# Performance work log

Hardware: AMD Instinct MI355X
Metric: run time of the kernel (lower is better)

## Reference

```python
import jax, jax.numpy as jnp
import numpy as np

N, E = 20000, 160000
D_NODE_IN, D_EDGE_IN = 256, 64
D = 128          # node/edge feature dim
H = 256          # edge hidden dim
T = 17           # number of keypoint types
EDGE_STEPS, NODE_STEPS = 2, 1


def _w(k, shape):
    return jax.random.normal(k, shape, dtype=jnp.float32) / np.sqrt(shape[-2] if len(shape) > 1 else shape[-1]).astype(np.float32)


def setup_inputs() -> dict:
    key = jax.random.key(0)
    ks = iter(jax.random.split(key, 40))
    inp = {
        'x': jax.random.normal(next(ks), (N, D_NODE_IN), dtype=jnp.float32),
        'edge_attr': jax.random.normal(next(ks), (E, D_EDGE_IN), dtype=jnp.float32),
        'edge_index': jax.random.randint(next(ks), (2, E), 0, N),
        'node_types': jax.random.randint(next(ks), (N,), 0, T),
        # type-routed node embedding: 17 stacked 2-layer MLPs 256->128->128
        'ne_w1': _w(next(ks), (T, D_NODE_IN, D)), 'ne_b1': jnp.zeros((T, D)),
        'ne_w2': _w(next(ks), (T, D, D)),         'ne_b2': jnp.zeros((T, D)),
        # edge embedding 64->128->128
        'ee_w1': _w(next(ks), (D_EDGE_IN, D)), 'ee_b1': jnp.zeros((D,)),
        'ee_w2': _w(next(ks), (D, D)),         'ee_b2': jnp.zeros((D,)),
        # MPLayer edge MLP: [x_i, x_j, e] with skip -> (2*2D + 2D)=768 -> 256 -> 128
        'me_w1': _w(next(ks), (4 * D + 2 * D, H)), 'me_b1': jnp.zeros((H,)),
        'me_w2': _w(next(ks), (H, D)),             'me_b2': jnp.zeros((D,)),
        # MPLayer node update: [x(skip 2D), agg(D)] -> 128
        'mn_w1': _w(next(ks), (2 * D + D, D)), 'mn_b1': jnp.zeros((D,)),
        # classifiers
        'ec_w1': _w(next(ks), (D, D)), 'ec_b1': jnp.zeros((D,)),
        'ec_w2': _w(next(ks), (D, 1)), 'ec_b2': jnp.zeros((1,)),
        'nc_w1': _w(next(ks), (D, D)), 'nc_b1': jnp.zeros((D,)),
        'nc_w2': _w(next(ks), (D, 1)), 'nc_b2': jnp.zeros((1,)),
        'cc_w1': _w(next(ks), (D, D)), 'cc_b1': jnp.zeros((D,)),
        'cc_w2': _w(next(ks), (D, T)), 'cc_b2': jnp.zeros((T,)),
    }
    return inp


def _mlp2(x, w1, b1, w2, b2):
    return jax.nn.relu(x @ w1 + b1) @ w2 + b2


def reference(x, edge_attr, edge_index, node_types,
              ne_w1, ne_b1, ne_w2, ne_b2,
              ee_w1, ee_b1, ee_w2, ee_b2,
              me_w1, me_b1, me_w2, me_b2,
              mn_w1, mn_b1,
              ec_w1, ec_b1, ec_w2, ec_b2,
              nc_w1, nc_b1, nc_w2, nc_b2,
              cc_w1, cc_b1, cc_w2, cc_b2):
    n = x.shape[0]
    # NodeMlpType: run all 17 MLPs, select by node type (same math as masked dispatch)
    h = jax.nn.relu(jnp.einsum('nd,tdk->tnk', x, ne_w1) + ne_b1[:, None, :])   # [T,N,D]
    o = jnp.einsum('tnk,tkm->tnm', h, ne_w2) + ne_b2[:, None, :]               # [T,N,D]
    nf0 = o[node_types, jnp.arange(n)]                                          # [N,D]
    ef0 = _mlp2(edge_attr, ee_w1, ee_b1, ee_w2, ee_b2)                          # [E,D]

    src, dst = edge_index[0], edge_index[1]

    def mp_step(nf, ef):
        nf_c = jnp.concatenate([nf0, nf], axis=1)                               # skip concat [N,2D]
        ef_c = jnp.concatenate([ef0, ef], axis=1)                               # [E,2D]
        m = jnp.concatenate([nf_c[dst], nf_c[src], ef_c], axis=1)               # [E,6D]
        e_new = _mlp2(m, me_w1, me_b1, me_w2, me_b2)                            # [E,D]
        agg = jax.ops.segment_sum(e_new, dst, num_segments=n)                   # aggr='add'
        nf_new = jnp.concatenate([nf_c, agg], axis=1) @ mn_w1 + mn_b1           # [N,D]
        return nf_new, e_new

    nf, ef = nf0, ef0
    for _ in range(EDGE_STEPS):
        nf, ef = mp_step(nf, ef)
    pred_edge = _mlp2(ef, ec_w1, ec_b1, ec_w2, ec_b2).squeeze(-1)               # [E]
    for _ in range(NODE_STEPS):
        nf, ef = mp_step(nf, ef)
    pred_node = _mlp2(nf, nc_w1, nc_b1, nc_w2, nc_b2).squeeze(-1)               # [N]
    pred_class = _mlp2(nf, cc_w1, cc_b1, cc_w2, cc_b2)                          # [N,T]
    return (pred_edge, pred_node, pred_class, nf, ef)
```

## Files before the change

### kernel.cpp

```cpp
#include <hip/hip_runtime.h>
#include <hip/hip_bf16.h>

#define N_NODES 20000
#define N_EDGES 160000
#define DIN_NODE 256
#define DIN_EDGE 64
#define DF 128
#define HH 256
#define TT 17
#define NE_PAD_SLOTS 20544
#define NB_NODE (NE_PAD_SLOTS / 32)

typedef __attribute__((ext_vector_type(8))) short short8v;
typedef __attribute__((ext_vector_type(4))) float f32x4;

__device__ __forceinline__ unsigned short f2bf(float f) {
  unsigned int u = __builtin_bit_cast(unsigned int, f);
  u += 0x7FFFu + ((u >> 16) & 1u);
  return (unsigned short)(u >> 16);
}

__device__ __forceinline__ float bf2f(unsigned short u) {
  return __builtin_bit_cast(float, (unsigned int)u << 16);
}

__device__ __forceinline__ short8v pack8(float4 a, float4 b) {
  short8v o;
  o[0] = (short)f2bf(a.x); o[1] = (short)f2bf(a.y);
  o[2] = (short)f2bf(a.z); o[3] = (short)f2bf(a.w);
  o[4] = (short)f2bf(b.x); o[5] = (short)f2bf(b.y);
  o[6] = (short)f2bf(b.z); o[7] = (short)f2bf(b.w);
  return o;
}

struct PackPtrs {
  const float *s0, *s1, *s2, *s3, *s4, *s5, *s6, *s7, *s8, *s9, *s10, *s11;
  unsigned short *d0, *d1, *d2, *d3, *d4, *d5, *d6, *d7, *d8, *d9, *d10, *d11;
};

__global__ __launch_bounds__(256) void k_pack_all(PackPtrs P) {
  const int g = blockIdx.x * 4 + (threadIdx.x >> 6);
  const int l = threadIdx.x & 63;
  if (g >= 2320) return;
  const float* w; unsigned short* out; int K, N, tile;
  if (g < 128)       { w = P.s0;  out = P.d0;  K = 256; N = 256; tile = g; }
  else if (g < 256)  { w = P.s1;  out = P.d1;  K = 256; N = 256; tile = g - 128; }
  else if (g < 384)  { w = P.s2;  out = P.d2;  K = 256; N = 256; tile = g - 256; }
  else if (g < 448)  { w = P.s3;  out = P.d3;  K = 256; N = 128; tile = g - 384; }
  else if (g < 544)  { w = P.s4;  out = P.d4;  K = 384; N = 128; tile = g - 448; }
  else if (g < 1632) { w = P.s5;  out = P.d5;  K = 256; N = 128; tile = g - 544; }
  else if (g < 2176) { w = P.s6;  out = P.d6;  K = 128; N = 128; tile = g - 1632; }
  else if (g < 2192) { w = P.s7;  out = P.d7;  K = 64;  N = 128; tile = g - 2176; }
  else if (g < 2224) { w = P.s8;  out = P.d8;  K = 128; N = 128; tile = g - 2192; }
  else if (g < 2256) { w = P.s9;  out = P.d9;  K = 128; N = 128; tile = g - 2224; }
  else if (g < 2288) { w = P.s10; out = P.d10; K = 128; N = 128; tile = g - 2256; }
  else               { w = P.s11; out = P.d11; K = 128; N = 128; tile = g - 2288; }
  const int ntTiles = N >> 4;
  const int tilesPer = (K >> 5) * ntTiles;
  const int bt = tile / tilesPer;
  const int rr = tile - bt * tilesPer;
  const int kt = rr / ntTiles, nt = rr - kt * ntTiles;
  const float* wb = w + (size_t)bt * K * N;
  const int col = (nt << 4) + (l & 15);
  const int k0 = (kt << 5) + ((l >> 4) << 3);
  unsigned short* o = out + (((size_t)tile << 6) + l) * 8;
#pragma unroll
  for (int j = 0; j < 8; ++j) o[j] = f2bf(wb[(size_t)(k0 + j) * N + col]);
}

__global__ void k_count_deg(const int* __restrict__ types,
                            const int* __restrict__ dstv,
                            int* __restrict__ cnt, int* __restrict__ deg) {
  const int i = blockIdx.x * 256 + threadIdx.x;
  if (i < N_NODES) atomicAdd(&cnt[types[i]], 1);
  if (i < N_EDGES) atomicAdd(&deg[dstv[i]], 1);
}

__global__ __launch_bounds__(256) void k_prefix_scan(
    const int* __restrict__ cnt, int* __restrict__ woff,
    const int* __restrict__ deg, int* __restrict__ rs, int* __restrict__ wo) {
  __shared__ int partial[256];
  const int t = threadIdx.x;
  if (t == 0) {
    int cur = 0;
    for (int ty = 0; ty < TT; ++ty) {
      woff[ty] = cur;
      cur += (cnt[ty] + 31) & ~31;
    }
  }
  const int base = t * 80;
  int s = 0;
  for (int j = 0; j < 80; ++j) {
    const int n = base + j;
    if (n < N_NODES) s += deg[n];
  }
  partial[t] = s;
  __syncthreads();
  for (int off = 1; off < 256; off <<= 1) {
    const int v = (t >= off) ? partial[t - off] : 0;
    __syncthreads();
    partial[t] += v;
    __syncthreads();
  }
  int run = (t > 0) ? partial[t - 1] : 0;
  for (int j = 0; j < 80; ++j) {
    const int n = base + j;
    if (n < N_NODES) {
      rs[n] = run; wo[n] = run;
      run += deg[n];
    }
  }
  if (t == 255) rs[N_NODES] = run;
}

__global__ void k_scatter_elist(const int* __restrict__ types,
                                const int* __restrict__ srcv,
                                const int* __restrict__ dstv,
                                int* __restrict__ woff, int* __restrict__ wo,
                                int* __restrict__ bucket,
                                int* __restrict__ elist, int* __restrict__ ipos,
                                int* __restrict__ srcp, int* __restrict__ dstp) {
  const int i = blockIdx.x * 256 + threadIdx.x;
  if (i < N_NODES) {
    const int pos = atomicAdd(&woff[types[i]], 1);
    bucket[pos] = i;
  }
  if (i < N_EDGES) {
    const int pos = atomicAdd(&wo[dstv[i]], 1);
    elist[pos] = i;
    ipos[i] = pos;
    srcp[pos] = srcv[i];
    dstp[pos] = dstv[i];
  }
}

__global__ __launch_bounds__(256) void k_embed_fused(
    const float* __restrict__ x, const int* __restrict__ bucket,
    const int* __restrict__ types,
    const unsigned short* __restrict__ wp1, const float* __restrict__ b1,
    const unsigned short* __restrict__ wp2, const float* __restrict__ b2,
    unsigned short* __restrict__ nf0b,
    const unsigned short* __restrict__ wpd, const unsigned short* __restrict__ wps,
    unsigned short* __restrict__ PDo, unsigned short* __restrict__ PSo,
    const float* __restrict__ ea, const int* __restrict__ ipos,
    const unsigned short* __restrict__ ewp1, const float* __restrict__ eb1,
    const unsigned short* __restrict__ ewp2, const float* __restrict__ eb2,
    unsigned short* __restrict__ ef0p) {
  __shared__ __align__(16) unsigned char A[32 * 512];
  __shared__ __align__(16) unsigned char Hb[32 * 256];
  __shared__ int sidx[32];
  const int t = threadIdx.x;
  const int w = t >> 6, l = t & 63, lr = l & 15, lg = l >> 4;
  const int sw = (lr & 7) << 4;
  const int row0 = lr, row1 = 16 + lr;

  if (blockIdx.x < NB_NODE) {
    const int r0 = blockIdx.x * 32;
    if (t < 32) sidx[t] = bucket[r0 + t];
    __syncthreads();
    if (sidx[0] < 0) return;
    const int ty = types[sidx[0]];

#pragma unroll
    for (int j = 0; j < 4; ++j) {
      const int q = j * 256 + t;
      const int i = q >> 5, c = q & 31;
      const int nd = sidx[i];
      short8v o;
      if (nd >= 0) {
        const float* xr = x + (size_t)nd * DIN_NODE + c * 8;
        o = pack8(*reinterpret_cast<const float4*>(xr),
                  *reinterpret_cast<const float4*>(xr + 4));
      } else {
#pragma unroll
        for (int k = 0; k < 8; ++k) o[k] = 0;
      }
      *reinterpret_cast<short8v*>(A + ((i * 512 + c * 16) ^ ((i & 7) << 4))) = o;
    }
    __syncthreads();

    f32x4 acc[2][2];
#pragma unroll
    for (int mt = 0; mt < 2; ++mt)
#pragma unroll
      for (int q = 0; q < 2; ++q)
#pragma unroll
        for (int r = 0; r < 4; ++r) acc[mt][q][r] = 0.f;
#pragma unroll
    for (int kt = 0; kt < 8; ++kt) {
      const short8v a0 = *reinterpret_cast<const short8v*>(
          A + ((row0 * 512 + kt * 64 + lg * 16) ^ sw));
      const short8v a1 = *reinterpret_cast<const short8v*>(
          A + ((row1 * 512 + kt * 64 + lg * 16) ^ sw));
#pragma unroll
      for (int q = 0; q < 2; ++q) {
// ... 104 lines not shown
    {
      const int i = t >> 3, c = t & 7;
      const float* xr = ea + (size_t)(e0 + i) * DIN_EDGE + c * 8;
      const short8v o = pack8(*reinterpret_cast<const float4*>(xr),
                              *reinterpret_cast<const float4*>(xr + 4));
      *reinterpret_cast<short8v*>(A + ((i * 128 + c * 16) ^ ((i & 7) << 4))) = o;
    }
    __syncthreads();

    f32x4 acc[2][2];
#pragma unroll
    for (int mt = 0; mt < 2; ++mt)
#pragma unroll
      for (int q = 0; q < 2; ++q)
#pragma unroll
        for (int r = 0; r < 4; ++r) acc[mt][q][r] = 0.f;
#pragma unroll
    for (int kt = 0; kt < 2; ++kt) {
      const short8v a0 = *reinterpret_cast<const short8v*>(
          A + ((row0 * 128 + kt * 64 + lg * 16) ^ sw));
      const short8v a1 = *reinterpret_cast<const short8v*>(
          A + ((row1 * 128 + kt * 64 + lg * 16) ^ sw));
#pragma unroll
      for (int q = 0; q < 2; ++q) {
        const short8v bq = *reinterpret_cast<const short8v*>(
            ewp1 + (((size_t)(kt * 8 + 2 * w + q) * 64 + l) << 3));
        acc[0][q] = __builtin_amdgcn_mfma_f32_16x16x32_bf16(a0, bq, acc[0][q], 0, 0, 0);
        acc[1][q] = __builtin_amdgcn_mfma_f32_16x16x32_bf16(a1, bq, acc[1][q], 0, 0, 0);
      }
    }
#pragma unroll
    for (int q = 0; q < 2; ++q) {
      const int col = (2 * w + q) * 16 + lr;
      const float bias = eb1[col];
#pragma unroll
      for (int mt = 0; mt < 2; ++mt)
#pragma unroll
        for (int r = 0; r < 4; ++r) {
          const int row = mt * 16 + lg * 4 + r;
          *reinterpret_cast<unsigned short*>(
              Hb + ((row * 256 + col * 2) ^ ((row & 7) << 4))) =
              f2bf(fmaxf(acc[mt][q][r] + bias, 0.f));
        }
    }
    __syncthreads();

    f32x4 acc2[2][2];
#pragma unroll
    for (int mt = 0; mt < 2; ++mt)
#pragma unroll
      for (int q = 0; q < 2; ++q)
#pragma unroll
        for (int r = 0; r < 4; ++r) acc2[mt][q][r] = 0.f;
#pragma unroll
    for (int kt = 0; kt < 4; ++kt) {
      const short8v a0 = *reinterpret_cast<const short8v*>(
          Hb + ((row0 * 256 + kt * 64 + lg * 16) ^ sw));
      const short8v a1 = *reinterpret_cast<const short8v*>(
          Hb + ((row1 * 256 + kt * 64 + lg * 16) ^ sw));
#pragma unroll
      for (int q = 0; q < 2; ++q) {
        const short8v bq = *reinterpret_cast<const short8v*>(
            ewp2 + (((size_t)(kt * 8 + 2 * w + q) * 64 + l) << 3));
        acc2[0][q] = __builtin_amdgcn_mfma_f32_16x16x32_bf16(a0, bq, acc2[0][q], 0, 0, 0);
        acc2[1][q] = __builtin_amdgcn_mfma_f32_16x16x32_bf16(a1, bq, acc2[1][q], 0, 0, 0);
      }
    }
#pragma unroll
    for (int q = 0; q < 2; ++q) {
      const int col = (2 * w + q) * 16 + lr;
      const float bias = eb2[col];
#pragma unroll
      for (int mt = 0; mt < 2; ++mt)
#pragma unroll
        for (int r = 0; r < 4; ++r) {
          const int row = mt * 16 + lg * 4 + r;
          ef0p[(size_t)sidx[row] * DF + col] = f2bf(acc2[mt][q][r] + bias);
        }
    }
  }
}

template <bool OUTF, bool HEAD>
__global__ __launch_bounds__(256, 4) void k_edge_mlp_mfma(
    const unsigned short* __restrict__ ef0, const unsigned short* __restrict__ ef_in,
    unsigned short* __restrict__ ef_out, float* __restrict__ ef_outf,
    const int* __restrict__ srcp, const int* __restrict__ dstp,
    const int* __restrict__ elist,
    const unsigned short* __restrict__ wpe, const float* __restrict__ b1,
    const unsigned short* __restrict__ wp2, const float* __restrict__ b2,
    const unsigned short* __restrict__ PDi, const unsigned short* __restrict__ PSi,
    const unsigned short* __restrict__ wech, const float* __restrict__ hb1,
    const float* __restrict__ hw2, const float* __restrict__ hb2,
    float* __restrict__ out_pe) {
  __shared__ __align__(16) unsigned char A_lds[32 * 512];
  __shared__ __align__(16) unsigned char P_lds[32 * 512];
  __shared__ int se[32];
  __shared__ float hpart[32][8];
  const int t = threadIdx.x;
  const int e0 = blockIdx.x * 32;
  if ((OUTF || HEAD) && t < 32) se[t] = elist[e0 + t];

  short8v av[4], pdv[4], psv[4];
#pragma unroll
  for (int j = 0; j < 4; ++j) {
    const int q = j * 256 + t;
    const int i = q >> 5, c = q & 31;
    const unsigned short* bp = (c < 16)
        ? ef0 + (size_t)(e0 + i) * DF + c * 8
        : ef_in + (size_t)(e0 + i) * DF + (c - 16) * 8;
    av[j] = *reinterpret_cast<const short8v*>(bp);
  }
#pragma unroll
  for (int j = 0; j < 4; ++j) {
    const int q = j * 256 + t;
    const int i = q >> 5, c = q & 31;
    const int dn = dstp[e0 + i];
    const int sn = srcp[e0 + i];
    pdv[j] = *reinterpret_cast<const short8v*>(PDi + (size_t)dn * HH + c * 8);
    psv[j] = *reinterpret_cast<const short8v*>(PSi + (size_t)sn * HH + c * 8);
  }
#pragma unroll
  for (int j = 0; j < 4; ++j) {
    const int q = j * 256 + t;
    const int i = q >> 5, c = q & 31;
    const int off = (i * 512 + c * 16) ^ ((i & 7) << 4);
    *reinterpret_cast<short8v*>(A_lds + off) = av[j];
    short8v o;
#pragma unroll
    for (int k = 0; k < 8; ++k)
      o[k] = (short)f2bf(bf2f((unsigned short)pdv[j][k]) +
                         bf2f((unsigned short)psv[j][k]));
    *reinterpret_cast<short8v*>(P_lds + off) = o;
  }
  __syncthreads();

  const int w = t >> 6, l = t & 63, lr = l & 15, lg = l >> 4;
  const int swz = (lr & 7) << 4;

  f32x4 acc[2][4];
#pragma unroll
  for (int mt = 0; mt < 2; ++mt)
#pragma unroll
    for (int q = 0; q < 4; ++q) {
      const int col = (4 * w + q) * 16 + lr;
#pragma unroll
      for (int r = 0; r < 4; ++r) {
        const int row = mt * 16 + lg * 4 + r;
        const unsigned short u = *reinterpret_cast<const unsigned short*>(
            P_lds + ((row * 512 + col * 2) ^ ((row & 7) << 4)));
        acc[mt][q][r] = bf2f(u);
      }
    }

  const int r0o = lr * 512 + lg * 16;
  const int r1o = (16 + lr) * 512 + lg * 16;
  const unsigned short* wb1 = wpe + (((size_t)(4 * w) * 64 + l) << 3);

  short8v aR[3][2], bR[3][4];
#pragma unroll
  for (int s = 0; s < 2; ++s) {
    aR[s][0] = *reinterpret_cast<const short8v*>(A_lds + ((r0o + s * 64) ^ swz));
    aR[s][1] = *reinterpret_cast<const short8v*>(A_lds + ((r1o + s * 64) ^ swz));
#pragma unroll
    for (int q = 0; q < 4; ++q)
      bR[s][q] = *reinterpret_cast<const short8v*>(wb1 + (size_t)s * 8192 + q * 512);
  }
#pragma unroll
  for (int kt = 0; kt < 8; ++kt) {
    const int cur = kt % 3, pf = (kt + 2) % 3;
    if (kt < 6) {
      aR[pf][0] = *reinterpret_cast<const short8v*>(
          A_lds + ((r0o + (kt + 2) * 64) ^ swz));
      aR[pf][1] = *reinterpret_cast<const short8v*>(
          A_lds + ((r1o + (kt + 2) * 64) ^ swz));
#pragma unroll
      for (int q = 0; q < 4; ++q)
        bR[pf][q] = *reinterpret_cast<const short8v*>(
            wb1 + (size_t)(kt + 2) * 8192 + q * 512);
    }
#pragma unroll
    for (int q = 0; q < 4; ++q) {
      acc[0][q] = __builtin_amdgcn_mfma_f32_16x16x32_bf16(aR[cur][0], bR[cur][q],
                                                          acc[0][q], 0, 0, 0);
      acc[1][q] = __builtin_amdgcn_mfma_f32_16x16x32_bf16(aR[cur][1], bR[cur][q],
                                                          acc[1][q], 0, 0, 0);
    }
  }
  __syncthreads();

#pragma unroll
  for (int q = 0; q < 4; ++q) {
    const int col = (4 * w + q) * 16 + lr;
    const float bias = b1[col];
#pragma unroll
    for (int mt = 0; mt < 2; ++mt)
#pragma unroll
      for (int r = 0; r < 4; ++r) {
        const int row = mt * 16 + lg * 4 + r;
        *reinterpret_cast<unsigned short*>(
            P_lds + ((row * 512 + col * 2) ^ ((row & 7) << 4))) =
            f2bf(fmaxf(acc[mt][q][r] + bias, 0.f));
      }
  }
  __syncthreads();

  f32x4 acc2[2][2];
#pragma unroll
  for (int mt = 0; mt < 2; ++mt)
#pragma unroll
    for (int q = 0; q < 2; ++q)
#pragma unroll
      for (int r = 0; r < 4; ++r) acc2[mt][q][r] = 0.f;

  const int h0o = lr * 512 + lg * 16;
  const int h1o = (16 + lr) * 512 + lg * 16;
  const unsigned short* wb2 = wp2 + (((size_t)(2 * w) * 64 + l) << 3);

  short8v aS[3][2], bS[3][2];
#pragma unroll
  for (int s = 0; s < 2; ++s) {
    aS[s][0] = *reinterpret_cast<const short8v*>(P_lds + ((h0o + s * 64) ^ swz));
    aS[s][1] = *reinterpret_cast<const short8v*>(P_lds + ((h1o + s * 64) ^ swz));
#pragma unroll
    for (int q = 0; q < 2; ++q)
      bS[s][q] = *reinterpret_cast<const short8v*>(wb2 + (size_t)s * 4096 + q * 512);
  }
#pragma unroll
  for (int kt = 0; kt < 8; ++kt) {
    const int cur = kt % 3, pf = (kt + 2) % 3;
    if (kt < 6) {
      aS[pf][0] = *reinterpret_cast<const short8v*>(
          P_lds + ((h0o + (kt + 2) * 64) ^ swz));
      aS[pf][1] = *reinterpret_cast<const short8v*>(
          P_lds + ((h1o + (kt + 2) * 64) ^ swz));
#pragma unroll
      for (int q = 0; q < 2; ++q)
        bS[pf][q] = *reinterpret_cast<const short8v*>(
            wb2 + (size_t)(kt + 2) * 4096 + q * 512);
    }
#pragma unroll
    for (int q = 0; q < 2; ++q) {
      acc2[0][q] = __builtin_amdgcn_mfma_f32_16x16x32_bf16(aS[cur][0], bS[cur][q],
                                                           acc2[0][q], 0, 0, 0);
      acc2[1][q] = __builtin_amdgcn_mfma_f32_16x16x32_bf16(aS[cur][1], bS[cur][q],
                                                           acc2[1][q], 0, 0, 0);
    }
  }

#pragma unroll
  for (int q = 0; q < 2; ++q) {
    const int n = (2 * w + q) * 16 + lr;
    const float bias = b2[n];
#pragma unroll
    for (int mt = 0; mt < 2; ++mt)
#pragma unroll
      for (int r = 0; r < 4; ++r) {
        const int m = mt * 16 + lg * 4 + r;
        const float v = acc2[mt][q][r] + bias;
        ef_out[(size_t)(e0 + m) * DF + n] = f2bf(v);
        if (OUTF)
          ef_outf[(size_t)se[m] * DF + n] = v;
      }
  }

  if constexpr (HEAD) {
    __syncthreads();
#pragma unroll
    for (int q = 0; q < 2; ++q) {
      const int n = (2 * w + q) * 16 + lr;
      const float bias = b2[n];
#pragma unroll
      for (int mt = 0; mt < 2; ++mt)
#pragma unroll
        for (int r = 0; r < 4; ++r) {
          const int m = mt * 16 + lg * 4 + r;
          *reinterpret_cast<unsigned short*>(
              P_lds + ((m * 256 + n * 2) ^ ((m & 7) << 4))) =
              f2bf(acc2[mt][q][r] + bias);
        }
    }
    __syncthreads();
    f32x4 ah[2][2];
#pragma unroll
    for (int mt = 0; mt < 2; ++mt)
#pragma unroll
      for (int q = 0; q < 2; ++q)
#pragma unroll
        for (int r = 0; r < 4; ++r) ah[mt][q][r] = 0.f;
#pragma unroll
    for (int kt = 0; kt < 4; ++kt) {
      const short8v a0 = *reinterpret_cast<const short8v*>(
          P_lds + ((lr * 256 + kt * 64 + lg * 16) ^ swz));
      const short8v a1 = *reinterpret_cast<const short8v*>(
          P_lds + (((16 + lr) * 256 + kt * 64 + lg * 16) ^ swz));
#pragma unroll
      for (int q = 0; q < 2; ++q) {
        const short8v bq = *reinterpret_cast<const short8v*>(
            wech + (((size_t)(kt * 8 + 2 * w + q) * 64 + l) << 3));
        ah[0][q] = __builtin_amdgcn_mfma_f32_16x16x32_bf16(a0, bq, ah[0][q], 0, 0, 0);
        ah[1][q] = __builtin_amdgcn_mfma_f32_16x16x32_bf16(a1, bq, ah[1][q], 0, 0, 0);
      }
    }
#pragma unroll
    for (int q = 0; q < 2; ++q) {
      const int col = (2 * w + q) * 16 + lr;
      const float bias = hb1[col];
#pragma unroll
      for (int mt = 0; mt < 2; ++mt)
#pragma unroll
        for (int r = 0; r < 4; ++r) {
          const int row = mt * 16 + lg * 4 + r;
          *reinterpret_cast<unsigned short*>(A_lds + row * 256 + col * 2) =
              f2bf(fmaxf(ah[mt][q][r] + bias, 0.f));
        }
    }
    __syncthreads();
    {
      const int rr = t >> 3, kc = t & 7;
      float s = 0.f;
#pragma unroll
      for (int u = 0; u < 16; ++u)
        s = fmaf(bf2f(*reinterpret_cast<const unsigned short*>(
                     A_lds + rr * 256 + (kc * 16 + u) * 2)),
                 hw2[kc * 16 + u], s);
      hpart[rr][kc] = s;
    }
    __syncthreads();
    if (t < 32) {
      float s = hb2[0];
#pragma unroll
      for (int k = 0; k < 8; ++k) s += hpart[t][k];
      out_pe[se[t]] = s;
    }
  }
}

template <bool OUTF, bool PART>
__global__ __launch_bounds__(256) void k_node_update_mfma(
    const unsigned short* __restrict__ nf0, const unsigned short* __restrict__ nfb,
    const unsigned short* __restrict__ efp,
    const int* __restrict__ rs, void* __restrict__ outp,
    const unsigned short* __restrict__ wp, const float* __restrict__ b,
    const unsigned short* __restrict__ wpd, const unsigned short* __restrict__ wps,
    unsigned short* __restrict__ PDo, unsigned short* __restrict__ PSo) {
  __shared__ __align__(16) unsigned char A[32 * 768];
  const int t = threadIdx.x;
  const int n0 = blockIdx.x * 32;
#pragma unroll
  for (int j = 0; j < 4; ++j) {
    const int q = j * 256 + t;
    const int i = q >> 5, c = q & 31;
    const unsigned short* bp = (c < 16)
        ? nf0 + (size_t)(n0 + i) * DF + c * 8
        : nfb + (size_t)(n0 + i) * DF + (c - 16) * 8;
    *reinterpret_cast<short8v*>(A + ((i * 768 + c * 16) ^ ((i & 7) << 4))) =
        *reinterpret_cast<const short8v*>(bp);
  }
  {
    const int i = t >> 3, sub = t & 7;
    const int n = n0 + i;
    const int kb = rs[n], ke = rs[n + 1];
    float av[16];
#pragma unroll
    for (int u = 0; u < 16; ++u) av[u] = 0.f;
    for (int k = kb; k < ke; ++k) {
      const unsigned short* er = efp + (size_t)k * DF + sub * 16;
      const short8v v0 = *reinterpret_cast<const short8v*>(er);
      const short8v v1 = *reinterpret_cast<const short8v*>(er + 8);
#pragma unroll
      for (int u = 0; u < 8; ++u) {
        av[u] += bf2f((unsigned short)v0[u]);
        av[8 + u] += bf2f((unsigned short)v1[u]);
      }
    }
    short8v o0, o1;
#pragma unroll
    for (int u = 0; u < 8; ++u) {
      o0[u] = (short)f2bf(av[u]);
      o1[u] = (short)f2bf(av[8 + u]);
    }
    const int c0 = 32 + sub * 2;
    *reinterpret_cast<short8v*>(A + ((i * 768 + c0 * 16) ^ ((i & 7) << 4))) = o0;
    *reinterpret_cast<short8v*>(A + ((i * 768 + (c0 + 1) * 16) ^ ((i & 7) << 4))) = o1;
  }
  __syncthreads();

  const int w = t >> 6, l = t & 63, lr = l & 15, lg = l >> 4;
  const int sw = (lr & 7) << 4;
  const int row0 = lr, row1 = 16 + lr;

  f32x4 acc[2][2];
#pragma unroll
  for (int mt = 0; mt < 2; ++mt)
#pragma unroll
    for (int q = 0; q < 2; ++q)
#pragma unroll
      for (int r = 0; r < 4; ++r) acc[mt][q][r] = 0.f;
#pragma unroll
  for (int kt = 0; kt < 12; ++kt) {
    const short8v a0 = *reinterpret_cast<const short8v*>(
        A + ((row0 * 768 + kt * 64 + lg * 16) ^ sw));
    const short8v a1 = *reinterpret_cast<const short8v*>(
        A + ((row1 * 768 + kt * 64 + lg * 16) ^ sw));
#pragma unroll
    for (int q = 0; q < 2; ++q) {
      const short8v bq = *reinterpret_cast<const short8v*>(
          wp + (((size_t)(kt * 8 + 2 * w + q) * 64 + l) << 3));
      acc[0][q] = __builtin_amdgcn_mfma_f32_16x16x32_bf16(a0, bq, acc[0][q], 0, 0, 0);
      acc[1][q] = __builtin_amdgcn_mfma_f32_16x16x32_bf16(a1, bq, acc[1][q], 0, 0, 0);
    }
  }
#pragma unroll
  for (int q = 0; q < 2; ++q) {
    const int col = (2 * w + q) * 16 + lr;
    const float bias = b[col];
#pragma unroll
    for (int mt = 0; mt < 2; ++mt)
#pragma unroll
      for (int r = 0; r < 4; ++r) {
        const int row = mt * 16 + lg * 4 + r;
        const float v = acc[mt][q][r] + bias;
        if (OUTF)
          ((float*)outp)[(size_t)(n0 + row) * DF + col] = v;
        else
          ((unsigned short*)outp)[(size_t)(n0 + row) * DF + col] = f2bf(v);
      }
  }

  if constexpr (PART) {
    __syncthreads();
#pragma unroll
    for (int q = 0; q < 2; ++q) {
      const int col = (2 * w + q) * 16 + lr;
      const float bias = b[col];
#pragma unroll
      for (int mt = 0; mt < 2; ++mt)
#pragma unroll
        for (int r = 0; r < 4; ++r) {
          const int row = mt * 16 + lg * 4 + r;
          *reinterpret_cast<unsigned short*>(
              A + ((row * 768 + 256 + col * 2) ^ ((row & 7) << 4))) =
              f2bf(acc[mt][q][r] + bias);
        }
    }
    __syncthreads();
    f32x4 aD[2][4], aSv[2][4];
#pragma unroll
    for (int mt = 0; mt < 2; ++mt)
#pragma unroll
      for (int q = 0; q < 4; ++q)
#pragma unroll
        for (int r = 0; r < 4; ++r) { aD[mt][q][r] = 0.f; aSv[mt][q][r] = 0.f; }
    const int r0p = lr * 768 + lg * 16, r1p = (16 + lr) * 768 + lg * 16;
#pragma unroll
    for (int kt = 0; kt < 8; ++kt) {
      const short8v a0 = *reinterpret_cast<const short8v*>(A + ((r0p + kt * 64) ^ sw));
      const short8v a1 = *reinterpret_cast<const short8v*>(A + ((r1p + kt * 64) ^ sw));
#pragma unroll
      for (int q = 0; q < 4; ++q) {
        const size_t bi = (((size_t)(kt * 16 + 4 * w + q) * 64 + l) << 3);
        const short8v bD = *reinterpret_cast<const short8v*>(wpd + bi);
        const short8v bSv = *reinterpret_cast<const short8v*>(wps + bi);
        aD[0][q] = __builtin_amdgcn_mfma_f32_16x16x32_bf16(a0, bD, aD[0][q], 0, 0, 0);
        aD[1][q] = __builtin_amdgcn_mfma_f32_16x16x32_bf16(a1, bD, aD[1][q], 0, 0, 0);
        aSv[0][q] = __builtin_amdgcn_mfma_f32_16x16x32_bf16(a0, bSv, aSv[0][q], 0, 0, 0);
        aSv[1][q] = __builtin_amdgcn_mfma_f32_16x16x32_bf16(a1, bSv, aSv[1][q], 0, 0, 0);
      }
    }
#pragma unroll
    for (int q = 0; q < 4; ++q) {
      const int col = (4 * w + q) * 16 + lr;
#pragma unroll
      for (int mt = 0; mt < 2; ++mt)
#pragma unroll
        for (int r = 0; r < 4; ++r) {
          const int row = mt * 16 + lg * 4 + r;
          PDo[(size_t)(n0 + row) * HH + col] = f2bf(aD[mt][q][r]);
          PSo[(size_t)(n0 + row) * HH + col] = f2bf(aSv[mt][q][r]);
        }
    }
  }
}

__global__ __launch_bounds__(256) void k_cls_both_mfma(
    const float* __restrict__ feat,
    const unsigned short* __restrict__ wpn, const float* __restrict__ nb1,
    const float* __restrict__ nw2, const float* __restrict__ nb2,
    const unsigned short* __restrict__ wpc, const float* __restrict__ cb1,
    const float* __restrict__ cw2, const float* __restrict__ cb2,
    float* __restrict__ out_pn, float* __restrict__ out_pc) {
  __shared__ __align__(16) unsigned char A[32 * 256];
  __shared__ float hid[32][136];
  __shared__ float w2s[DF * TT];
  __shared__ float nw2s[DF];
  __shared__ float part[32][8];
  const int t = threadIdx.x;
  const int r0 = blockIdx.x * 32;
  for (int j = t; j < DF * TT; j += 256) w2s[j] = cw2[j];
  if (t < DF) nw2s[t] = nw2[t];
#pragma unroll
  for (int j = 0; j < 2; ++j) {
    const int q = j * 256 + t;
    const int i = q >> 4, c = q & 15;
    const float* fr = feat + (size_t)(r0 + i) * DF + c * 8;
    const short8v o = pack8(*reinterpret_cast<const float4*>(fr),
                            *reinterpret_cast<const float4*>(fr + 4));
    *reinterpret_cast<short8v*>(A + ((i * 256 + c * 16) ^ ((i & 7) << 4))) = o;
  }
  __syncthreads();

  const int w = t >> 6, l = t & 63, lr = l & 15, lg = l >> 4;
  const int sw = (lr & 7) << 4;
  const int row0 = lr, row1 = 16 + lr;

  f32x4 acc[2][2];
#pragma unroll
  for (int mt = 0; mt < 2; ++mt)
#pragma unroll
    for (int q = 0; q < 2; ++q)
#pragma unroll
      for (int r = 0; r < 4; ++r) acc[mt][q][r] = 0.f;
#pragma unroll
  for (int kt = 0; kt < 4; ++kt) {
    const short8v a0 = *reinterpret_cast<const short8v*>(
        A + ((row0 * 256 + kt * 64 + lg * 16) ^ sw));
    const short8v a1 = *reinterpret_cast<const short8v*>(
        A + ((row1 * 256 + kt * 64 + lg * 16) ^ sw));
#pragma unroll
    for (int q = 0; q < 2; ++q) {
      const short8v bq = *reinterpret_cast<const short8v*>(
          wpn + (((size_t)(kt * 8 + 2 * w + q) * 64 + l) << 3));
      acc[0][q] = __builtin_amdgcn_mfma_f32_16x16x32_bf16(a0, bq, acc[0][q], 0, 0, 0);
      acc[1][q] = __builtin_amdgcn_mfma_f32_16x16x32_bf16(a1, bq, acc[1][q], 0, 0, 0);
    }
  }
#pragma unroll
  for (int q = 0; q < 2; ++q) {
    const int col = (2 * w + q) * 16 + lr;
    const float bias = nb1[col];
#pragma unroll
    for (int mt = 0; mt < 2; ++mt)
#pragma unroll
      for (int r = 0; r < 4; ++r) {
        const int row = mt * 16 + lg * 4 + r;
        hid[row][col] = fmaxf(acc[mt][q][r] + bias, 0.f);
      }
  }
  __syncthreads();
  {
    const int r = t >> 3, kc = t & 7;
    float s = 0.f;
#pragma unroll
    for (int u = 0; u < 16; ++u) s = fmaf(hid[r][kc * 16 + u], nw2s[kc * 16 + u], s);
    part[r][kc] = s;
  }
  __syncthreads();
  if (t < 32) {
    float s = nb2[0];
#pragma unroll
    for (int k = 0; k < 8; ++k) s += part[t][k];
    out_pn[r0 + t] = s;
  }
  __syncthreads();

  f32x4 acc2[2][2];
#pragma unroll
  for (int mt = 0; mt < 2; ++mt)
#pragma unroll
    for (int q = 0; q < 2; ++q)
#pragma unroll
      for (int r = 0; r < 4; ++r) acc2[mt][q][r] = 0.f;
#pragma unroll
  for (int kt = 0; kt < 4; ++kt) {
    const short8v a0 = *reinterpret_cast<const short8v*>(
        A + ((row0 * 256 + kt * 64 + lg * 16) ^ sw));
    const short8v a1 = *reinterpret_cast<const short8v*>(
        A + ((row1 * 256 + kt * 64 + lg * 16) ^ sw));
#pragma unroll
    for (int q = 0; q < 2; ++q) {
      const short8v bq = *reinterpret_cast<const short8v*>(
          wpc + (((size_t)(kt * 8 + 2 * w + q) * 64 + l) << 3));
      acc2[0][q] = __builtin_amdgcn_mfma_f32_16x16x32_bf16(a0, bq, acc2[0][q], 0, 0, 0);
      acc2[1][q] = __builtin_amdgcn_mfma_f32_16x16x32_bf16(a1, bq, acc2[1][q], 0, 0, 0);
    }
  }
#pragma unroll
  for (int q = 0; q < 2; ++q) {
    const int col = (2 * w + q) * 16 + lr;
    const float bias = cb1[col];
#pragma unroll
    for (int mt = 0; mt < 2; ++mt)
#pragma unroll
      for (int r = 0; r < 4; ++r) {
        const int row = mt * 16 + lg * 4 + r;
        hid[row][col] = fmaxf(acc2[mt][q][r] + bias, 0.f);
      }
  }
  __syncthreads();
  for (int o = t; o < 32 * TT; o += 256) {
    const int r = o / TT, c = o - TT * r;
    float s = cb2[c];
    for (int k = 0; k < DF; ++k) s = fmaf(hid[r][k], w2s[k * TT + c], s);
    out_pc[(size_t)(r0 + r) * TT + c] = s;
  }
}

extern "C" void kernel_launch(void* const* d_in, const int* in_sizes, int n_in,
                              void* d_out, int out_size, void* d_ws,
                              size_t ws_size, hipStream_t stream) {
  (void)in_sizes; (void)n_in; (void)out_size; (void)ws_size;
  const float* x         = (const float*)d_in[0];
  const float* edge_attr = (const float*)d_in[1];
  const int*   edge_idx  = (const int*)d_in[2];
  const int*   node_ty   = (const int*)d_in[3];
  const float* ne_w1 = (const float*)d_in[4];
  const float* ne_b1 = (const float*)d_in[5];
  const float* ne_w2 = (const float*)d_in[6];
  const float* ne_b2 = (const float*)d_in[7];
  const float* ee_w1 = (const float*)d_in[8];
  const float* ee_b1 = (const float*)d_in[9];
  const float* ee_w2 = (const float*)d_in[10];
  const float* ee_b2 = (const float*)d_in[11];
  const float* me_w1 = (const float*)d_in[12];
  const float* me_b1 = (const float*)d_in[13];
  const float* me_w2 = (const float*)d_in[14];
  const float* me_b2 = (const float*)d_in[15];
  const float* mn_w1 = (const float*)d_in[16];
  const float* mn_b1 = (const float*)d_in[17];
  const float* ec_w1 = (const float*)d_in[18];
  const float* ec_b1 = (const float*)d_in[19];
  const float* ec_w2 = (const float*)d_in[20];
  const float* ec_b2 = (const float*)d_in[21];
  const float* nc_w1 = (const float*)d_in[22];
  const float* nc_b1 = (const float*)d_in[23];
  const float* nc_w2 = (const float*)d_in[24];
  const float* nc_b2 = (const float*)d_in[25];
  const float* cc_w1 = (const float*)d_in[26];
  const float* cc_b1 = (const float*)d_in[27];
  const float* cc_w2 = (const float*)d_in[28];
  const float* cc_b2 = (const float*)d_in[29];

  const int* srcv = edge_idx;
  const int* dstv = edge_idx + N_EDGES;

  unsigned short* nf0b = (unsigned short*)d_ws;
  unsigned short* nf1b = nf0b + (size_t)N_NODES * DF;
  unsigned short* ef0p = nf1b + (size_t)N_NODES * DF;
  unsigned short* ef1p = ef0p + (size_t)N_EDGES * DF;
  unsigned short* wmpD = ef1p + (size_t)N_EDGES * DF;
  unsigned short* wmpS = wmpD + 256 * 256;
  unsigned short* wmeE = wmpS + 256 * 256;
  unsigned short* wme2 = wmeE + 256 * 256;
  unsigned short* wmn  = wme2 + 256 * 128;
  unsigned short* wne1 = wmn + 384 * 128;
  unsigned short* wne2 = wne1 + (size_t)TT * 256 * 128;
  unsigned short* wee1 = wne2 + (size_t)TT * 128 * 128;
  unsigned short* wee2 = wee1 + 64 * 128;
  unsigned short* wec  = wee2 + 128 * 128;
  unsigned short* wnc  = wec + 128 * 128;
  unsigned short* wcc  = wnc + 128 * 128;
  unsigned short* PD   = wcc + 128 * 128;
  unsigned short* PS   = PD + (size_t)N_NODES * HH;
  int* cnt    = (int*)(PS + (size_t)N_NODES * HH);
  int* woff   = cnt + 32;
  int* bucket = woff + 32;
  int* deg    = bucket + NE_PAD_SLOTS;
  int* rs     = deg + N_NODES;
  int* wo     = rs + N_NODES + 1;
  int* elist  = wo + N_NODES;
  int* ipos   = elist + N_EDGES;
  int* srcp   = ipos + N_EDGES;
  int* dstp   = srcp + N_EDGES;

  float* out_pe = (float*)d_out;
  float* out_pn = out_pe + N_EDGES;
  float* out_pc = out_pn + N_NODES;
  float* out_nf = out_pc + (size_t)N_NODES * TT;
  float* out_ef = out_nf + (size_t)N_NODES * DF;

  PackPtrs P;
  P.s0 = me_w1;            P.d0 = wmpD;
  P.s1 = me_w1 + 256*256;  P.d1 = wmpS;
  P.s2 = me_w1 + 512*256;  P.d2 = wmeE;
  P.s3 = me_w2;            P.d3 = wme2;
  P.s4 = mn_w1;            P.d4 = wmn;
  P.s5 = ne_w1;            P.d5 = wne1;
  P.s6 = ne_w2;            P.d6 = wne2;
  P.s7 = ee_w1;            P.d7 = wee1;
  P.s8 = ee_w2;            P.d8 = wee2;
  P.s9 = ec_w1;            P.d9 = wec;
  P.s10 = nc_w1;           P.d10 = wnc;
  P.s11 = cc_w1;           P.d11 = wcc;
  k_pack_all<<<580, 256, 0, stream>>>(P);

  hipMemsetAsync(cnt, 0, 32 * sizeof(int), stream);
  hipMemsetAsync(deg, 0, N_NODES * sizeof(int), stream);
  hipMemsetAsync(bucket, 0xFF, NE_PAD_SLOTS * sizeof(int), stream);
  k_count_deg<<<(N_EDGES + 255) / 256, 256, 0, stream>>>(node_ty, dstv, cnt, deg);
  k_prefix_scan<<<1, 256, 0, stream>>>(cnt, woff, deg, rs, wo);
  k_scatter_elist<<<(N_EDGES + 255) / 256, 256, 0, stream>>>(
      node_ty, srcv, dstv, woff, wo, bucket, elist, ipos, srcp, dstp);

  k_embed_fused<<<NB_NODE + N_EDGES / 32, 256, 0, stream>>>(
      x, bucket, node_ty, wne1, ne_b1, wne2, ne_b2, nf0b, wmpD, wmpS, PD, PS,
      edge_attr, ipos, wee1, ee_b1, wee2, ee_b2, ef0p);

  k_edge_mlp_mfma<false, false><<<N_EDGES / 32, 256, 0, stream>>>(
      ef0p, ef0p, ef1p, nullptr, srcp, dstp, elist, wmeE, me_b1, wme2, me_b2,
      PD, PS, nullptr, nullptr, nullptr, nullptr, nullptr);
  k_node_update_mfma<false, true><<<N_NODES / 32, 256, 0, stream>>>(
      nf0b, nf0b, ef1p, rs, (void*)nf1b, wmn, mn_b1, wmpD, wmpS, PD, PS);
  k_edge_mlp_mfma<false, true><<<N_EDGES / 32, 256, 0, stream>>>(
      ef0p, ef1p, ef1p, nullptr, srcp, dstp, elist, wmeE, me_b1, wme2, me_b2,
      PD, PS, wec, ec_b1, ec_w2, ec_b2, out_pe);
  k_node_update_mfma<false, true><<<N_NODES / 32, 256, 0, stream>>>(
      nf0b, nf1b, ef1p, rs, (void*)nf1b, wmn, mn_b1, wmpD, wmpS, PD, PS);
  k_edge_mlp_mfma<true, false><<<N_EDGES / 32, 256, 0, stream>>>(
      ef0p, ef1p, ef1p, out_ef, srcp, dstp, elist, wmeE, me_b1, wme2, me_b2,
      PD, PS, nullptr, nullptr, nullptr, nullptr, nullptr);
  k_node_update_mfma<true, false><<<N_NODES / 32, 256, 0, stream>>>(
      nf0b, nf1b, ef1p, rs, (void*)out_nf, wmn, mn_b1, wmpD, wmpS, PD, PS);

  k_cls_both_mfma<<<N_NODES / 32, 256, 0, stream>>>(
      out_nf, wnc, nc_b1, nc_w2, nc_b2, wcc, cc_b1, cc_w2, cc_b2, out_pn,
      out_pc);
}
```

Before: 554.5 us.

## Fuse node and class heads into final node update; widen prefix scan

The separate classifier kernel is removed and its two head MLPs now run inside the last node-update kernel, using the accumulators already in registers and reusing the kernel's shared memory. This avoids one launch and the re-read of the float node features. The prefix scan now uses 1024 threads so each thread handles fewer serial elements. The edge MLP occupancy hint is raised from 4 to 5 blocks, and edge-list indices are loaded into registers instead of shared memory. The risks are that bf16 rounding of the hidden activations and of cw2 changes the head numerics, and that the tighter occupancy bound may cause register spills.

```diff
diff --git a/kernel.cpp b/kernel.cpp
--- a/kernel.cpp
+++ b/kernel.cpp
@@ -76,10 +76,10 @@
   if (i < N_EDGES) atomicAdd(&deg[dstv[i]], 1);
 }
 
-__global__ __launch_bounds__(256) void k_prefix_scan(
+__global__ __launch_bounds__(1024) void k_prefix_scan(
     const int* __restrict__ cnt, int* __restrict__ woff,
     const int* __restrict__ deg, int* __restrict__ rs, int* __restrict__ wo) {
-  __shared__ int partial[256];
+  __shared__ int partial[1024];
   const int t = threadIdx.x;
   if (t == 0) {
     int cur = 0;
@@ -88,29 +88,29 @@
       cur += (cnt[ty] + 31) & ~31;
     }
   }
-  const int base = t * 80;
+  const int base = t * 20;
   int s = 0;
-  for (int j = 0; j < 80; ++j) {
+  for (int j = 0; j < 20; ++j) {
     const int n = base + j;
     if (n < N_NODES) s += deg[n];
   }
   partial[t] = s;
   __syncthreads();
-  for (int off = 1; off < 256; off <<= 1) {
+  for (int off = 1; off < 1024; off <<= 1) {
     const int v = (t >= off) ? partial[t - off] : 0;
     __syncthreads();
     partial[t] += v;
     __syncthreads();
   }
   int run = (t > 0) ? partial[t - 1] : 0;
-  for (int j = 0; j < 80; ++j) {
+  for (int j = 0; j < 20; ++j) {
     const int n = base + j;
     if (n < N_NODES) {
       rs[n] = run; wo[n] = run;
       run += deg[n];
     }
   }
-  if (t == 255) rs[N_NODES] = run;
+  if (t == 1023) rs[N_NODES] = run;
 }
 
 __global__ void k_scatter_elist(const int* __restrict__ types,
@@ -381,7 +381,7 @@
 }
 
 template <bool OUTF, bool HEAD>
-__global__ __launch_bounds__(256, 4) void k_edge_mlp_mfma(
+__global__ __launch_bounds__(256, 5) void k_edge_mlp_mfma(
     const unsigned short* __restrict__ ef0, const unsigned short* __restrict__ ef_in,
     unsigned short* __restrict__ ef_out, float* __restrict__ ef_outf,
     const int* __restrict__ srcp, const int* __restrict__ dstp,
@@ -394,11 +394,8 @@
     float* __restrict__ out_pe) {
   __shared__ __align__(16) unsigned char A_lds[32 * 512];
   __shared__ __align__(16) unsigned char P_lds[32 * 512];
-  __shared__ int se[32];
-  __shared__ float hpart[32][8];
   const int t = threadIdx.x;
   const int e0 = blockIdx.x * 32;
-  if ((OUTF || HEAD) && t < 32) se[t] = elist[e0 + t];
 
   short8v av[4], pdv[4], psv[4];
 #pragma unroll
@@ -547,6 +544,14 @@
     }
   }
 
+  int seL[2][4];
+  if constexpr (OUTF) {
+#pragma unroll
+    for (int mt = 0; mt < 2; ++mt)
+#pragma unroll
+      for (int r = 0; r < 4; ++r)
+        seL[mt][r] = elist[e0 + mt * 16 + lg * 4 + r];
+  }
 #pragma unroll
   for (int q = 0; q < 2; ++q) {
     const int n = (2 * w + q) * 16 + lr;
@@ -559,11 +564,12 @@
         const float v = acc2[mt][q][r] + bias;
         ef_out[(size_t)(e0 + m) * DF + n] = f2bf(v);
         if (OUTF)
-          ef_outf[(size_t)se[m] * DF + n] = v;
+          ef_outf[(size_t)seL[mt][r] * DF + n] = v;
       }
   }
 
   if constexpr (HEAD) {
+    __shared__ float hpart[32][8];
     __syncthreads();
 #pragma unroll
     for (int q = 0; q < 2; ++q) {
@@ -630,19 +636,24 @@
       float s = hb2[0];
 #pragma unroll
       for (int k = 0; k < 8; ++k) s += hpart[t][k];
-      out_pe[se[t]] = s;
+      out_pe[elist[e0 + t]] = s;
     }
   }
 }
 
-template <bool OUTF, bool PART>
+template <bool OUTF, bool PART, bool HEADS>
 __global__ __launch_bounds__(256) void k_node_update_mfma(
     const unsigned short* __restrict__ nf0, const unsigned short* __restrict__ nfb,
     const unsigned short* __restrict__ efp,
     const int* __restrict__ rs, void* __restrict__ outp,
     const unsigned short* __restrict__ wp, const float* __restrict__ b,
     const unsigned short* __restrict__ wpd, const unsigned short* __restrict__ wps,
-    unsigned short* __restrict__ PDo, unsigned short* __restrict__ PSo) {
+    unsigned short* __restrict__ PDo, unsigned short* __restrict__ PSo,
+    const unsigned short* __restrict__ wpn, const float* __restrict__ nb1,
+    const float* __restrict__ nw2, const float* __restrict__ nb2,
+    const unsigned short* __restrict__ wpc, const float* __restrict__ cb1,
+    const float* __restrict__ cw2, const float* __restrict__ cb2,
+    float* __restrict__ out_pn, float* __restrict__ out_pc) {
   __shared__ __align__(16) unsigned char A[32 * 768];
   const int t = threadIdx.x;
   const int n0 = blockIdx.x * 32;
@@ -780,128 +791,121 @@
         }
     }
   }
-}
-
-__global__ __launch_bounds__(256) void k_cls_both_mfma(
-    const float* __restrict__ feat,
-    const unsigned short* __restrict__ wpn, const float* __restrict__ nb1,
-    const float* __restrict__ nw2, const float* __restrict__ nb2,
-    const unsigned short* __restrict__ wpc, const float* __restrict__ cb1,
-    const float* __restrict__ cw2, const float* __restrict__ cb2,
-    float* __restrict__ out_pn, float* __restrict__ out_pc) {
-  __shared__ __align__(16) unsigned char A[32 * 256];
-  __shared__ float hid[32][136];
-  __shared__ float w2s[DF * TT];
-  __shared__ float nw2s[DF];
-  __shared__ float part[32][8];
-  const int t = threadIdx.x;
-  const int r0 = blockIdx.x * 32;
-  for (int j = t; j < DF * TT; j += 256) w2s[j] = cw2[j];
-  if (t < DF) nw2s[t] = nw2[t];
-#pragma unroll
-  for (int j = 0; j < 2; ++j) {
-    const int q = j * 256 + t;
-    const int i = q >> 4, c = q & 15;
-    const float* fr = feat + (size_t)(r0 + i) * DF + c * 8;
-    const short8v o = pack8(*reinterpret_cast<const float4*>(fr),
-                            *reinterpret_cast<const float4*>(fr + 4));
-    *reinterpret_cast<short8v*>(A + ((i * 256 + c * 16) ^ ((i & 7) << 4))) = o;
-  }
-  __syncthreads();
-
-  const int w = t >> 6, l = t & 63, lr = l & 15, lg = l >> 4;
-  const int sw = (lr & 7) << 4;
-  const int row0 = lr, row1 = 16 + lr;
-
-  f32x4 acc[2][2];
-#pragma unroll
-  for (int mt = 0; mt < 2; ++mt)
-#pragma unroll
-    for (int q = 0; q < 2; ++q)
-#pragma unroll
-      for (int r = 0; r < 4; ++r) acc[mt][q][r] = 0.f;
-#pragma unroll
-  for (int kt = 0; kt < 4; ++kt) {
-    const short8v a0 = *reinterpret_cast<const short8v*>(
-        A + ((row0 * 256 + kt * 64 + lg * 16) ^ sw));
-    const short8v a1 = *reinterpret_cast<const short8v*>(
-        A + ((row1 * 256 + kt * 64 + lg * 16) ^ sw));
-#pragma unroll
-    for (int q = 0; q < 2; ++q) {
-      const short8v bq = *reinterpret_cast<const short8v*>(
-          wpn + (((size_t)(kt * 8 + 2 * w + q) * 64 + l) << 3));
-      acc[0][q] = __builtin_amdgcn_mfma_f32_16x16x32_bf16(a0, bq, acc[0][q], 0, 0, 0);
-      acc[1][q] = __builtin_amdgcn_mfma_f32_16x16x32_bf16(a1, bq, acc[1][q], 0, 0, 0);
-    }
-  }
-#pragma unroll
-  for (int q = 0; q < 2; ++q) {
-    const int col = (2 * w + q) * 16 + lr;
-    const float bias = nb1[col];
-#pragma unroll
-    for (int mt = 0; mt < 2; ++mt)
-#pragma unroll
-      for (int r = 0; r < 4; ++r) {
-        const int row = mt * 16 + lg * 4 + r;
-        hid[row][col] = fmaxf(acc[mt][q][r] + bias, 0.f);
-      }
-  }
-  __syncthreads();
-  {
-    const int r = t >> 3, kc = t & 7;
-    float s = 0.f;
-#pragma unroll
-    for (int u = 0; u < 16; ++u) s = fmaf(hid[r][kc * 16 + u], nw2s[kc * 16 + u], s);
-    part[r][kc] = s;
-  }
-  __syncthreads();
-  if (t < 32) {
-    float s = nb2[0];
-#pragma unroll
-    for (int k = 0; k < 8; ++k) s += part[t][k];
-    out_pn[r0 + t] = s;
-  }
-  __syncthreads();
-
-  f32x4 acc2[2][2];
-#pragma unroll
-  for (int mt = 0; mt < 2; ++mt)
-#pragma unroll
-    for (int q = 0; q < 2; ++q)
-#pragma unroll
-      for (int r = 0; r < 4; ++r) acc2[mt][q][r] = 0.f;
-#pragma unroll
-  for (int kt = 0; kt < 4; ++kt) {
-    const short8v a0 = *reinterpret_cast<const short8v*>(
-        A + ((row0 * 256 + kt * 64 + lg * 16) ^ sw));
-    const short8v a1 = *reinterpret_cast<const short8v*>(
-        A + ((row1 * 256 + kt * 64 + lg * 16) ^ sw));
-#pragma unroll
-    for (int q = 0; q < 2; ++q) {
-      const short8v bq = *reinterpret_cast<const short8v*>(
-          wpc + (((size_t)(kt * 8 + 2 * w + q) * 64 + l) << 3));
-      acc2[0][q] = __builtin_amdgcn_mfma_f32_16x16x32_bf16(a0, bq, acc2[0][q], 0, 0, 0);
-      acc2[1][q] = __builtin_amdgcn_mfma_f32_16x16x32_bf16(a1, bq, acc2[1][q], 0, 0, 0);
-    }
-  }
-#pragma unroll
-  for (int q = 0; q < 2; ++q) {
-    const int col = (2 * w + q) * 16 + lr;
-    const float bias = cb1[col];
-#pragma unroll
-    for (int mt = 0; mt < 2; ++mt)
-#pragma unroll
-      for (int r = 0; r < 4; ++r) {
-        const int row = mt * 16 + lg * 4 + r;
-        hid[row][col] = fmaxf(acc2[mt][q][r] + bias, 0.f);
-      }
-  }
-  __syncthreads();
-  for (int o = t; o < 32 * TT; o += 256) {
-    const int r = o / TT, c = o - TT * r;
-    float s = cb2[c];
-    for (int k = 0; k < DF; ++k) s = fmaf(hid[r][k], w2s[k * TT + c], s);
-    out_pc[(size_t)(r0 + r) * TT + c] = s;
+
+  if constexpr (HEADS) {
+    __syncthreads();
+    unsigned short* cw2b = reinterpret_cast<unsigned short*>(A + 17408);
+    for (int j = t; j < DF * TT; j += 256) cw2b[j] = f2bf(cw2[j]);
+#pragma unroll
+    for (int q = 0; q < 2; ++q) {
+      const int col = (2 * w + q) * 16 + lr;
+      const float bias = b[col];
+#pragma unroll
+      for (int mt = 0; mt < 2; ++mt)
+#pragma unroll
+        for (int r = 0; r < 4; ++r) {
+          const int row = mt * 16 + lg * 4 + r;
+          *reinterpret_cast<unsigned short*>(
+              A + ((row * 256 + col * 2) ^ ((row & 7) << 4))) =
+              f2bf(acc[mt][q][r] + bias);
+        }
+    }
+    __syncthreads();
+
+    f32x4 ah[2][2];
+#pragma unroll
+    for (int mt = 0; mt < 2; ++mt)
+#pragma unroll
+      for (int q = 0; q < 2; ++q)
+#pragma unroll
+        for (int r = 0; r < 4; ++r) ah[mt][q][r] = 0.f;
+#pragma unroll
+    for (int kt = 0; kt < 4; ++kt) {
+      const short8v a0 = *reinterpret_cast<const short8v*>(
+          A + ((row0 * 256 + kt * 64 + lg * 16) ^ sw));
+      const short8v a1 = *reinterpret_cast<const short8v*>(
+          A + ((row1 * 256 + kt * 64 + lg * 16) ^ sw));
+#pragma unroll
+      for (int q = 0; q < 2; ++q) {
+        const short8v bq = *reinterpret_cast<const short8v*>(
+            wpn + (((size_t)(kt * 8 + 2 * w + q) * 64 + l) << 3));
+        ah[0][q] = __builtin_amdgcn_mfma_f32_16x16x32_bf16(a0, bq, ah[0][q], 0, 0, 0);
+        ah[1][q] = __builtin_amdgcn_mfma_f32_16x16x32_bf16(a1, bq, ah[1][q], 0, 0, 0);
+      }
+    }
+    unsigned short* hid = reinterpret_cast<unsigned short*>(A + 8192);
+#pragma unroll
+    for (int q = 0; q < 2; ++q) {
+      const int col = (2 * w + q) * 16 + lr;
+      const float bias = nb1[col];
+#pragma unroll
+      for (int mt = 0; mt < 2; ++mt)
+#pragma unroll
+        for (int r = 0; r < 4; ++r) {
+          const int row = mt * 16 + lg * 4 + r;
+          hid[row * 128 + col] = f2bf(fmaxf(ah[mt][q][r] + bias, 0.f));
+        }
+    }
+    __syncthreads();
+    float* part = reinterpret_cast<float*>(A + 16384);
+    {
+      const int rr = t >> 3, kc = t & 7;
+      float s = 0.f;
+#pragma unroll
+      for (int u = 0; u < 16; ++u)
+        s = fmaf(bf2f(hid[rr * 128 + kc * 16 + u]), nw2[kc * 16 + u], s);
+      part[rr * 8 + kc] = s;
+    }
+    __syncthreads();
+    if (t < 32) {
+      float s = nb2[0];
+#pragma unroll
+      for (int k = 0; k < 8; ++k) s += part[t * 8 + k];
+      out_pn[n0 + t] = s;
+    }
+    __syncthreads();
+
+    f32x4 ac2[2][2];
+#pragma unroll
+    for (int mt = 0; mt < 2; ++mt)
+#pragma unroll
+      for (int q = 0; q < 2; ++q)
+#pragma unroll
+        for (int r = 0; r < 4; ++r) ac2[mt][q][r] = 0.f;
+#pragma unroll
+    for (int kt = 0; kt < 4; ++kt) {
+      const short8v a0 = *reinterpret_cast<const short8v*>(
+          A + ((row0 * 256 + kt * 64 + lg * 16) ^ sw));
+      const short8v a1 = *reinterpret_cast<const short8v*>(
+          A + ((row1 * 256 + kt * 64 + lg * 16) ^ sw));
+#pragma unroll
+      for (int q = 0; q < 2; ++q) {
+        const short8v bq = *reinterpret_cast<const short8v*>(
+            wpc + (((size_t)(kt * 8 + 2 * w + q) * 64 + l) << 3));
+        ac2[0][q] = __builtin_amdgcn_mfma_f32_16x16x32_bf16(a0, bq, ac2[0][q], 0, 0, 0);
+        ac2[1][q] = __builtin_amdgcn_mfma_f32_16x16x32_bf16(a1, bq, ac2[1][q], 0, 0, 0);
+      }
+    }
+#pragma unroll
+    for (int q = 0; q < 2; ++q) {
+      const int col = (2 * w + q) * 16 + lr;
+      const float bias = cb1[col];
+#pragma unroll
+      for (int mt = 0; mt < 2; ++mt)
+#pragma unroll
+        for (int r = 0; r < 4; ++r) {
+          const int row = mt * 16 + lg * 4 + r;
+          hid[row * 128 + col] = f2bf(fmaxf(ac2[mt][q][r] + bias, 0.f));
+        }
+    }
+    __syncthreads();
+    for (int o = t; o < 32 * TT; o += 256) {
+      const int rr = o / TT, c = o - TT * rr;
+      float s = cb2[c];
+      for (int k = 0; k < DF; ++k)
+        s = fmaf(bf2f(hid[rr * 128 + k]), bf2f(cw2b[k * TT + c]), s);
+      out_pc[(size_t)(n0 + rr) * TT + c] = s;
+    }
   }
 }
 
@@ -997,7 +1001,7 @@
   hipMemsetAsync(deg, 0, N_NODES * sizeof(int), stream);
   hipMemsetAsync(bucket, 0xFF, NE_PAD_SLOTS * sizeof(int), stream);
   k_count_deg<<<(N_EDGES + 255) / 256, 256, 0, stream>>>(node_ty, dstv, cnt, deg);
-  k_prefix_scan<<<1, 256, 0, stream>>>(cnt, woff, deg, rs, wo);
+  k_prefix_scan<<<1, 1024, 0, stream>>>(cnt, woff, deg, rs, wo);
   k_scatter_elist<<<(N_EDGES + 255) / 256, 256, 0, stream>>>(
       node_ty, srcv, dstv, woff, wo, bucket, elist, ipos, srcp, dstp);
 
@@ -1008,20 +1012,21 @@
   k_edge_mlp_mfma<false, false><<<N_EDGES / 32, 256, 0, stream>>>(
       ef0p, ef0p, ef1p, nullptr, srcp, dstp, elist, wmeE, me_b1, wme2, me_b2,
       PD, PS, nullptr, nullptr, nullptr, nullptr, nullptr);
-  k_node_update_mfma<false, true><<<N_NODES / 32, 256, 0, stream>>>(
-      nf0b, nf0b, ef1p, rs, (void*)nf1b, wmn, mn_b1, wmpD, wmpS, PD, PS);
+  k_node_update_mfma<false, true, false><<<N_NODES / 32, 256, 0, stream>>>(
+      nf0b, nf0b, ef1p, rs, (void*)nf1b, wmn, mn_b1, wmpD, wmpS, PD, PS,
+      nullptr, nullptr, nullptr, nullptr, nullptr, nullptr, nullptr, nullptr,
+      nullptr, nullptr);
   k_edge_mlp_mfma<false, true><<<N_EDGES / 32, 256, 0, stream>>>(
       ef0p, ef1p, ef1p, nullptr, srcp, dstp, elist, wmeE, me_b1, wme2, me_b2,
       PD, PS, wec, ec_b1, ec_w2, ec_b2, out_pe);
-  k_node_update_mfma<false, true><<<N_NODES / 32, 256, 0, stream>>>(
-      nf0b, nf1b, ef1p, rs, (void*)nf1b, wmn, mn_b1, wmpD, wmpS, PD, PS);
+  k_node_update_mfma<false, true, false><<<N_NODES / 32, 256, 0, stream>>>(
+      nf0b, nf1b, ef1p, rs, (void*)nf1b, wmn, mn_b1, wmpD, wmpS, PD, PS,
+      nullptr, nullptr, nullptr, nullptr, nullptr, nullptr, nullptr, nullptr,
+      nullptr, nullptr);
   k_edge_mlp_mfma<true, false><<<N_EDGES / 32, 256, 0, stream>>>(
       ef0p, ef1p, ef1p, out_ef, srcp, dstp, elist, wmeE, me_b1, wme2, me_b2,
       PD, PS, nullptr, nullptr, nullptr, nullptr, nullptr);
-  k_node_update_mfma<true, false><<<N_NODES / 32, 256, 0, stream>>>(
-      nf0b, nf1b, ef1p, rs, (void*)out_nf, wmn, mn_b1, wmpD, wmpS, PD, PS);
-
-  k_cls_both_mfma<<<N_NODES / 32, 256, 0, stream>>>(
-      out_nf, wnc, nc_b1, nc_w2, nc_b2, wcc, cc_b1, cc_w2, cc_b2, out_pn,
-      out_pc);
+  k_node_update_mfma<true, false, true><<<N_NODES / 32, 256, 0, stream>>>(
+      nf0b, nf1b, ef1p, rs, (void*)out_nf, wmn, mn_b1, wmpD, wmpS, PD, PS,
+      wnc, nc_b1, nc_w2, nc_b2, wcc, cc_b1, cc_w2, cc_b2, out_pn, out_pc);
 }
```

Result: no change. 561.9 us (+1.3%).
